# Kernel optimization log

Measured on AMD Instinct MI355X. Metric: run time of the kernel, lower is better.

The kernel has to match this reference:

```python
import jax, jax.numpy as jnp
import numpy as np

N_EMBD = 1024
N_HEAD = 16
B, T = 4, 2048

def setup_inputs() -> dict:
    key = jax.random.key(0)
    ks = jax.random.split(key, 5)
    s_attn = 1.0 / np.sqrt(N_EMBD)
    s_proj = 1.0 / np.sqrt(N_EMBD)
    return {
        "x": jax.random.normal(ks[0], (B, T, N_EMBD), dtype=jnp.float32),
        "w_attn": jax.random.uniform(ks[1], (N_EMBD, 3 * N_EMBD), jnp.float32, -s_attn, s_attn),
        "b_attn": jax.random.uniform(ks[2], (3 * N_EMBD,), jnp.float32, -s_attn, s_attn),
        "w_proj": jax.random.uniform(ks[3], (N_EMBD, N_EMBD), jnp.float32, -s_proj, s_proj),
        "b_proj": jax.random.uniform(ks[4], (N_EMBD,), jnp.float32, -s_proj, s_proj),
    }

def reference(x, w_attn, b_attn, w_proj, b_proj):
    Bx, Tx, C = x.shape
    hd = C // N_HEAD  # head dim
    qkv = x @ w_attn + b_attn                       # [B,T,3C]
    q, k, v = jnp.split(qkv, 3, axis=-1)
    # [B,T,C] -> [B,H,T,hd]
    def heads(t):
        return t.reshape(Bx, Tx, N_HEAD, hd).transpose(0, 2, 1, 3)
    q, k, v = heads(q), heads(k), heads(v)
    att = jnp.einsum('bhqd,bhkd->bhqk', q, k) * (1.0 / np.sqrt(hd))
    causal = jnp.tril(jnp.ones((Tx, Tx), dtype=bool))
    att = jnp.where(causal, att, -jnp.inf)
    att = jax.nn.softmax(att, axis=-1)
    y = jnp.einsum('bhqk,bhkd->bhqd', att, v)       # [B,H,T,hd]
    y = y.transpose(0, 2, 1, 3).reshape(Bx, Tx, C)
    return y @ w_proj + b_proj
```

## Files before the change

### kernel.cpp

```cpp
#include <hip/hip_runtime.h>
#include <cstdint>

typedef unsigned short u16;
typedef short s16x8 __attribute__((ext_vector_type(8)));
typedef short s16x4 __attribute__((ext_vector_type(4)));
typedef float f32x4 __attribute__((ext_vector_type(4)));

#define B_   4
#define T_   2048
#define C_   1024
#define H_   16
#define HD_  64
#define M_   8192
#define N3_  3072

#define QSCALE 0.18033688011112042f

__device__ inline u16 f2b(float f) {
  union { float f; uint32_t u; } v; v.f = f;
  uint32_t u = v.u;
  return (u16)((u + 0x7FFFu + ((u >> 16) & 1u)) >> 16);
}

__device__ inline uint32_t cvtpk(float lo, float hi) {
  uint32_t r;
  asm("v_cvt_pk_bf16_f32 %0, %1, %2" : "=v"(r) : "v"(lo), "v"(hi));
  return r;
}

__device__ inline f32x4 mfma16(s16x4 a, s16x4 b, f32x4 c) {
#if __has_builtin(__builtin_amdgcn_mfma_f32_16x16x16bf16_1k)
  return __builtin_amdgcn_mfma_f32_16x16x16bf16_1k(a, b, c, 0, 0, 0);
#else
  f32x4 d;
  asm("v_mfma_f32_16x16x16_bf16 %0, %1, %2, %3"
      : "=v"(d) : "v"(a), "v"(b), "v"(c));
  return d;
#endif
}

__device__ inline void gload_lds16(const void* g, void* l) {
  __builtin_amdgcn_global_load_lds(
      (const __attribute__((address_space(1))) void*)g,
      (__attribute__((address_space(3))) void*)l, 16, 0, 0);
}

__global__ __launch_bounds__(256) void cvt_f32_bf16(
    const float* __restrict__ in, u16* __restrict__ out, int n) {
  int i = (blockIdx.x * 256 + threadIdx.x) * 8;
  if (i >= n) return;
  float4 a = *(const float4*)(in + i);
  float4 b = *(const float4*)(in + i + 4);
  s16x8 r;
  r[0] = (short)f2b(a.x); r[1] = (short)f2b(a.y);
  r[2] = (short)f2b(a.z); r[3] = (short)f2b(a.w);
  r[4] = (short)f2b(b.x); r[5] = (short)f2b(b.y);
  r[6] = (short)f2b(b.z); r[7] = (short)f2b(b.w);
  *(s16x8*)(out + i) = r;
}

__global__ __launch_bounds__(256) void cvt_transpose(
    const float* __restrict__ W, u16* __restrict__ WT, int K, int N) {
  __shared__ u16 tile[64][65];
  int n0 = blockIdx.x * 64, k0 = blockIdx.y * 64;
  int j = threadIdx.x & 63, i0 = threadIdx.x >> 6;
#pragma unroll
  for (int i = i0; i < 64; i += 4)
    tile[i][j] = f2b(W[(size_t)(k0 + i) * N + n0 + j]);
  __syncthreads();
#pragma unroll
  for (int i = i0; i < 64; i += 4)
    WT[(size_t)(n0 + i) * K + k0 + j] = tile[j][i];
}

template <int MODE>
__global__ __launch_bounds__(256, 4) void gemm_bt(
    const u16* __restrict__ A, const u16* __restrict__ Bt,
    const float* __restrict__ bias, float* __restrict__ outf,
    u16* __restrict__ qo, u16* __restrict__ ko, u16* __restrict__ vo,
    int M, int N, int K) {
  __shared__ u16 As[128 * 64];
  __shared__ u16 Bs[128 * 64];

  int nwg = gridDim.x;
  int bid0 = blockIdx.x;
  int bid = (bid0 & 7) * (nwg >> 3) + (bid0 >> 3);
  int nbn = N >> 7;
  int bm = bid / nbn, bn = bid % nbn;
  int m0 = bm * 128, n0 = bn * 128;
  int tid = threadIdx.x;
  int lane = tid & 63, w = tid >> 6;
  int wm = (w >> 1) * 64, wn = (w & 1) * 64;
  int l15 = lane & 15, g = lane >> 4;

  f32x4 acc[4][4] = {};

  for (int kb = 0; kb < K; kb += 64) {
    __syncthreads();
#pragma unroll
    for (int p = 0; p < 4; ++p) {
      int idx = p * 256 + tid;
      int row = idx >> 3, pc = idx & 7;
      int sc = (pc ^ (row & 7)) * 8;
      gload_lds16(A  + (size_t)(m0 + row) * K + kb + sc, &As[idx * 8]);
      gload_lds16(Bt + (size_t)(n0 + row) * K + kb + sc, &Bs[idx * 8]);
    }
    __syncthreads();

#pragma unroll
    for (int ks = 0; ks < 2; ++ks) {
      int ck = ((g + 4 * ks) ^ (l15 & 7)) * 8;
      s16x8 af[4], bf[4];
#pragma unroll
      for (int mi = 0; mi < 4; ++mi)
        af[mi] = *(const s16x8*)&As[(wm + mi * 16 + l15) * 64 + ck];
#pragma unroll
      for (int ni = 0; ni < 4; ++ni)
        bf[ni] = *(const s16x8*)&Bs[(wn + ni * 16 + l15) * 64 + ck];
#pragma unroll
      for (int mi = 0; mi < 4; ++mi)
#pragma unroll
        for (int ni = 0; ni < 4; ++ni)
          acc[mi][ni] = __builtin_amdgcn_mfma_f32_16x16x32_bf16(
              af[mi], bf[ni], acc[mi][ni], 0, 0, 0);
    }
  }

#pragma unroll
  for (int mi = 0; mi < 4; ++mi)
#pragma unroll
    for (int ni = 0; ni < 4; ++ni) {
      int col = n0 + wn + ni * 16 + l15;
      float bv = bias[col];
      int row0 = m0 + wm + mi * 16 + g * 4;
      if (MODE == 0) {
#pragma unroll
        for (int r = 0; r < 4; ++r)
          outf[(size_t)(row0 + r) * N + col] = acc[mi][ni][r] + bv;
      } else {
        int which = col >> 10, hc = col & 1023;
        int h = hc >> 6, d = hc & 63;
        int b = row0 >> 11, t0 = row0 & 2047;
        if (which == 2) {
          s16x4 pv;
#pragma unroll
          for (int r = 0; r < 4; ++r) pv[r] = (short)f2b(acc[mi][ni][r] + bv);
          *(s16x4*)(vo + ((size_t)((b * 16 + h) * 64 + d)) * 2048 + t0) = pv;
        } else {
          u16* dst = (which == 0) ? qo : ko;
          float sc2 = (which == 0) ? QSCALE : 1.0f;
#pragma unroll
          for (int r = 0; r < 4; ++r)
            dst[(((size_t)(b * 16 + h)) * 2048 + (t0 + r)) * 64 + d] =
                f2b((acc[mi][ni][r] + bv) * sc2);
        }
      }
    }
}

__global__ __launch_bounds__(256, 4) void attn_fwd(
    const u16* __restrict__ Q, const u16* __restrict__ Kg,
    const u16* __restrict__ Vt, u16* __restrict__ Y) {
  __shared__ u16 Ks[64 * 64];
  __shared__ u16 Vs[64 * 64];

  int bid = blockIdx.x;
  int bh = bid & 63;
  int qt = 31 - (bid >> 6);
  int tid = threadIdx.x, lane = tid & 63, w = tid >> 6;
  int l15 = lane & 15, g = lane >> 4;

  const u16* Qh = Q  + (size_t)bh * T_ * HD_;
  const u16* Kh = Kg + (size_t)bh * T_ * HD_;
  const u16* Vh = Vt + (size_t)bh * HD_ * T_;

  int q0 = qt * 64 + w * 16;
  int qrow = q0 + l15;

  s16x8 qa[2];
#pragma unroll
  for (int ks = 0; ks < 2; ++ks)
    qa[ks] = *(const s16x8*)(Qh + (size_t)qrow * HD_ + g * 8 + ks * 32);

  f32x4 oacc[4] = {};
  float m = -3.0e30f, l = 0.f;

  int sr = tid >> 3, sc = tid & 7;
  int wswz = (sr & 7) << 4;
  int rswz = (l15 & 7) << 4;
  char* KsB = (char*)Ks;
  char* VsB = (char*)Vs;

  s16x8 kr0 = *(const s16x8*)(Kh + (size_t)sr * HD_ + sc * 8);
  s16x8 kr1 = *(const s16x8*)(Kh + (size_t)(sr + 32) * HD_ + sc * 8);
  s16x8 vr0 = *(const s16x8*)(Vh + (size_t)sr * T_ + sc * 8);
  s16x8 vr1 = *(const s16x8*)(Vh + (size_t)(sr + 32) * T_ + sc * 8);

  int ntile = qt + 1;
  for (int kt = 0; kt < ntile; ++kt) {
    int kvb = kt * 64;
    __syncthreads();
    *(s16x8*)(KsB + sr * 128 + ((sc * 16) ^ wswz))        = kr0;
    *(s16x8*)(KsB + (sr + 32) * 128 + ((sc * 16) ^ wswz)) = kr1;
    *(s16x8*)(VsB + sr * 128 + ((sc * 16) ^ wswz))        = vr0;
    *(s16x8*)(VsB + (sr + 32) * 128 + ((sc * 16) ^ wswz)) = vr1;
    __syncthreads();

    {
      int kvn = (kt + 1 < ntile) ? (kt + 1) * 64 : 0;
      kr0 = *(const s16x8*)(Kh + (size_t)(kvn + sr) * HD_ + sc * 8);
      kr1 = *(const s16x8*)(Kh + (size_t)(kvn + sr + 32) * HD_ + sc * 8);
      vr0 = *(const s16x8*)(Vh + (size_t)sr * T_ + kvn + sc * 8);
      vr1 = *(const s16x8*)(Vh + (size_t)(sr + 32) * T_ + kvn + sc * 8);
    }

    f32x4 sacc[4] = {};
    __builtin_amdgcn_s_setprio(1);
#pragma unroll
    for (int cf = 0; cf < 4; ++cf)
#pragma unroll
      for (int ks = 0; ks < 2; ++ks) {
        s16x8 kb = *(const s16x8*)(KsB + (cf * 16 + l15) * 128 +
                                   ((g * 16 + ks * 64) ^ rswz));
        sacc[cf] = __builtin_amdgcn_mfma_f32_16x16x32_bf16(kb, qa[ks], sacc[cf], 0, 0, 0);
      }
    __builtin_amdgcn_s_setprio(0);

    if (kt == qt) {
#pragma unroll
      for (int cf = 0; cf < 4; ++cf)
#pragma unroll
        for (int r = 0; r < 4; ++r) {
          int kv = kvb + cf * 16 + g * 4 + r;
          if (kv > qrow) sacc[cf][r] = -1e30f;
        }
    }

    float t0 = fmaxf(fmaxf(sacc[0][0], sacc[0][1]), fmaxf(sacc[0][2], sacc[0][3]));
    float t1 = fmaxf(fmaxf(sacc[1][0], sacc[1][1]), fmaxf(sacc[1][2], sacc[1][3]));
    float t2 = fmaxf(fmaxf(sacc[2][0], sacc[2][1]), fmaxf(sacc[2][2], sacc[2][3]));
    float t3 = fmaxf(fmaxf(sacc[3][0], sacc[3][1]), fmaxf(sacc[3][2], sacc[3][3]));
    float mx = fmaxf(fmaxf(t0, t1), fmaxf(t2, t3));
    mx = fmaxf(mx, __shfl_xor(mx, 16, 64));
    mx = fmaxf(mx, __shfl_xor(mx, 32, 64));

    if (!__all(mx <= m + 8.0f)) {
      float mn = fmaxf(m, mx);
      float alpha = __builtin_amdgcn_exp2f(m - mn);
      m = mn;
      l *= alpha;
#pragma unroll
      for (int df = 0; df < 4; ++df)
#pragma unroll
        for (int r = 0; r < 4; ++r) oacc[df][r] *= alpha;
    }

    float rs = 0.f;
#pragma unroll
    for (int cf = 0; cf < 4; ++cf)
#pragma unroll
      for (int r = 0; r < 4; ++r) {
        float p = __builtin_amdgcn_exp2f(sacc[cf][r] - m);
        sacc[cf][r] = p;
        rs += p;
      }
    rs += __shfl_xor(rs, 16, 64);
    rs += __shfl_xor(rs, 32, 64);
    l += rs;

#pragma unroll
    for (int cf = 0; cf < 4; ++cf) {
      union { uint32_t u[2]; s16x4 v; } pk;
      pk.u[0] = cvtpk(sacc[cf][0], sacc[cf][1]);
      pk.u[1] = cvtpk(sacc[cf][2], sacc[cf][3]);
      __builtin_amdgcn_s_setprio(1);
#pragma unroll
      for (int df = 0; df < 4; ++df) {
        s16x4 va = *(const s16x4*)(VsB + (df * 16 + l15) * 128 +
                                   ((cf * 32 + g * 8) ^ rswz));
        oacc[df] = mfma16(va, pk.v, oacc[df]);
      }
      __builtin_amdgcn_s_setprio(0);
    }
  }

  int b = bh >> 4, h = bh & 15;
  float inv = 1.0f / l;
  u16* yrow = Y + ((size_t)b * T_ + qrow) * C_ + h * 64;
#pragma unroll
  for (int df = 0; df < 4; ++df) {
    union { uint32_t u[2]; s16x4 v; } pk;
    pk.u[0] = cvtpk(oacc[df][0] * inv, oacc[df][1] * inv);
    pk.u[1] = cvtpk(oacc[df][2] * inv, oacc[df][3] * inv);
    *(s16x4*)(yrow + df * 16 + g * 4) = pk.v;
  }
}

extern "C" void kernel_launch(void* const* d_in, const int* in_sizes, int n_in,
                              void* d_out, int out_size, void* d_ws, size_t ws_size,
                              hipStream_t stream) {
  const float* x      = (const float*)d_in[0];
  const float* w_attn = (const float*)d_in[1];
  const float* b_attn = (const float*)d_in[2];
  const float* w_proj = (const float*)d_in[3];
  const float* b_proj = (const float*)d_in[4];
  float* out = (float*)d_out;

  u16* ws  = (u16*)d_ws;
  u16* xb  = ws;
  u16* wat = xb  + (size_t)M_ * C_;
  u16* wpt = wat + (size_t)N3_ * C_;
  u16* q   = wpt + (size_t)C_ * C_;
  u16* k   = q   + (size_t)M_ * C_;
  u16* v   = k   + (size_t)M_ * C_;
  u16* ya  = xb;

  cvt_f32_bf16<<<dim3((M_ * C_) / (256 * 8)), dim3(256), 0, stream>>>(x, xb, M_ * C_);
  cvt_transpose<<<dim3(N3_ / 64, C_ / 64), dim3(256), 0, stream>>>(w_attn, wat, C_, N3_);
  cvt_transpose<<<dim3(C_ / 64, C_ / 64), dim3(256), 0, stream>>>(w_proj, wpt, C_, C_);

  gemm_bt<1><<<dim3((M_ / 128) * (N3_ / 128)), dim3(256), 0, stream>>>(
      xb, wat, b_attn, nullptr, q, k, v, M_, N3_, C_);

  attn_fwd<<<dim3(64 * 32), dim3(256), 0, stream>>>(q, k, v, ya);

  gemm_bt<0><<<dim3((M_ / 128) * (C_ / 128)), dim3(256), 0, stream>>>(
      ya, wpt, b_proj, out, nullptr, nullptr, nullptr, M_, C_, C_);
}
```

Baseline: 186.5 us.

## Switch attention to 32x32x16 MFMA with 128-row query blocks per workgroup

Rewrites the attention kernel so each workgroup handles 128 query rows (32 per wave) instead of 64, and uses 32x32x16 bf16 MFMAs for both QK^T and PV in place of 16x16 variants. Each K/V tile loaded into LDS is therefore reused by twice as many queries, and P is repacked across lane halves with shuffles to form the B operand for PV. Waves whose query rows lie entirely before a KV tile skip its compute. The cost is more accumulator registers (occupancy hint lowered from 4 to 3 workgroups per CU), half as many workgroups, and extra shuffle work per tile.

```diff
diff --git a/kernel.cpp b/kernel.cpp
--- a/kernel.cpp
+++ b/kernel.cpp
@@ -5,6 +5,7 @@
 typedef short s16x8 __attribute__((ext_vector_type(8)));
 typedef short s16x4 __attribute__((ext_vector_type(4)));
 typedef float f32x4 __attribute__((ext_vector_type(4)));
+typedef float f32x16 __attribute__((ext_vector_type(16)));
 
 #define B_   4
 #define T_   2048
@@ -26,17 +27,6 @@
   uint32_t r;
   asm("v_cvt_pk_bf16_f32 %0, %1, %2" : "=v"(r) : "v"(lo), "v"(hi));
   return r;
-}
-
-__device__ inline f32x4 mfma16(s16x4 a, s16x4 b, f32x4 c) {
-#if __has_builtin(__builtin_amdgcn_mfma_f32_16x16x16bf16_1k)
-  return __builtin_amdgcn_mfma_f32_16x16x16bf16_1k(a, b, c, 0, 0, 0);
-#else
-  f32x4 d;
-  asm("v_mfma_f32_16x16x16_bf16 %0, %1, %2, %3"
-      : "=v"(d) : "v"(a), "v"(b), "v"(c));
-  return d;
-#endif
 }
 
 __device__ inline void gload_lds16(const void* g, void* l) {
@@ -158,7 +148,7 @@
     }
 }
 
-__global__ __launch_bounds__(256, 4) void attn_fwd(
+__global__ __launch_bounds__(256, 3) void attn_fwd(
     const u16* __restrict__ Q, const u16* __restrict__ Kg,
     const u16* __restrict__ Vt, u16* __restrict__ Y) {
   __shared__ u16 Ks[64 * 64];
@@ -166,28 +156,29 @@
 
   int bid = blockIdx.x;
   int bh = bid & 63;
-  int qt = 31 - (bid >> 6);
+  int qb = 15 - (bid >> 6);
   int tid = threadIdx.x, lane = tid & 63, w = tid >> 6;
-  int l15 = lane & 15, g = lane >> 4;
+  int l31 = lane & 31, half = lane >> 5;
 
   const u16* Qh = Q  + (size_t)bh * T_ * HD_;
   const u16* Kh = Kg + (size_t)bh * T_ * HD_;
   const u16* Vh = Vt + (size_t)bh * HD_ * T_;
 
-  int q0 = qt * 64 + w * 16;
-  int qrow = q0 + l15;
-
-  s16x8 qa[2];
-#pragma unroll
-  for (int ks = 0; ks < 2; ++ks)
-    qa[ks] = *(const s16x8*)(Qh + (size_t)qrow * HD_ + g * 8 + ks * 32);
-
-  f32x4 oacc[4] = {};
+  int q0 = qb * 128;
+  int qw = q0 + w * 32;
+  int qrow = qw + l31;
+
+  s16x8 qa[4];
+#pragma unroll
+  for (int kst = 0; kst < 4; ++kst)
+    qa[kst] = *(const s16x8*)(Qh + (size_t)qrow * HD_ + kst * 16 + half * 8);
+
+  f32x16 oacc[2] = {};
   float m = -3.0e30f, l = 0.f;
 
   int sr = tid >> 3, sc = tid & 7;
   int wswz = (sr & 7) << 4;
-  int rswz = (l15 & 7) << 4;
+  int rswz = (l31 & 7) << 4;
   char* KsB = (char*)Ks;
   char* VsB = (char*)Vs;
 
@@ -196,7 +187,7 @@
   s16x8 vr0 = *(const s16x8*)(Vh + (size_t)sr * T_ + sc * 8);
   s16x8 vr1 = *(const s16x8*)(Vh + (size_t)(sr + 32) * T_ + sc * 8);
 
-  int ntile = qt + 1;
+  int ntile = 2 * qb + 2;
   for (int kt = 0; kt < ntile; ++kt) {
     int kvb = kt * 64;
     __syncthreads();
@@ -214,34 +205,40 @@
       vr1 = *(const s16x8*)(Vh + (size_t)(sr + 32) * T_ + kvn + sc * 8);
     }
 
-    f32x4 sacc[4] = {};
+    if (kvb > qw + 31) continue;
+
+    f32x16 s0 = {}, s1 = {};
     __builtin_amdgcn_s_setprio(1);
 #pragma unroll
-    for (int cf = 0; cf < 4; ++cf)
-#pragma unroll
-      for (int ks = 0; ks < 2; ++ks) {
-        s16x8 kb = *(const s16x8*)(KsB + (cf * 16 + l15) * 128 +
-                                   ((g * 16 + ks * 64) ^ rswz));
-        sacc[cf] = __builtin_amdgcn_mfma_f32_16x16x32_bf16(kb, qa[ks], sacc[cf], 0, 0, 0);
+    for (int kst = 0; kst < 4; ++kst) {
+      s16x8 kb0 = *(const s16x8*)(KsB +
+          (((l31) * 128 + kst * 32 + half * 16) ^ rswz));
+      s0 = __builtin_amdgcn_mfma_f32_32x32x16_bf16(kb0, qa[kst], s0, 0, 0, 0);
+      s16x8 kb1 = *(const s16x8*)(KsB +
+          (((32 + l31) * 128 + kst * 32 + half * 16) ^ rswz));
+      s1 = __builtin_amdgcn_mfma_f32_32x32x16_bf16(kb1, qa[kst], s1, 0, 0, 0);
+    }
+    __builtin_amdgcn_s_setprio(0);
+
+    if (kvb + 63 > qw) {
+#pragma unroll
+      for (int r = 0; r < 16; ++r) {
+        int kv0 = kvb + (r & 3) + 8 * (r >> 2) + 4 * half;
+        if (kv0 > qrow) s0[r] = -1e30f;
+        if (kv0 + 32 > qrow) s1[r] = -1e30f;
       }
-    __builtin_amdgcn_s_setprio(0);
-
-    if (kt == qt) {
-#pragma unroll
-      for (int cf = 0; cf < 4; ++cf)
-#pragma unroll
-        for (int r = 0; r < 4; ++r) {
-          int kv = kvb + cf * 16 + g * 4 + r;
-          if (kv > qrow) sacc[cf][r] = -1e30f;
-        }
-    }
-
-    float t0 = fmaxf(fmaxf(sacc[0][0], sacc[0][1]), fmaxf(sacc[0][2], sacc[0][3]));
-    float t1 = fmaxf(fmaxf(sacc[1][0], sacc[1][1]), fmaxf(sacc[1][2], sacc[1][3]));
-    float t2 = fmaxf(fmaxf(sacc[2][0], sacc[2][1]), fmaxf(sacc[2][2], sacc[2][3]));
-    float t3 = fmaxf(fmaxf(sacc[3][0], sacc[3][1]), fmaxf(sacc[3][2], sacc[3][3]));
-    float mx = fmaxf(fmaxf(t0, t1), fmaxf(t2, t3));
-    mx = fmaxf(mx, __shfl_xor(mx, 16, 64));
+    }
+
+    float a0 = fmaxf(fmaxf(s0[0], s0[1]), fmaxf(s0[2], s0[3]));
+    float a1 = fmaxf(fmaxf(s0[4], s0[5]), fmaxf(s0[6], s0[7]));
+    float a2 = fmaxf(fmaxf(s0[8], s0[9]), fmaxf(s0[10], s0[11]));
+    float a3 = fmaxf(fmaxf(s0[12], s0[13]), fmaxf(s0[14], s0[15]));
+    float a4 = fmaxf(fmaxf(s1[0], s1[1]), fmaxf(s1[2], s1[3]));
+    float a5 = fmaxf(fmaxf(s1[4], s1[5]), fmaxf(s1[6], s1[7]));
+    float a6 = fmaxf(fmaxf(s1[8], s1[9]), fmaxf(s1[10], s1[11]));
+    float a7 = fmaxf(fmaxf(s1[12], s1[13]), fmaxf(s1[14], s1[15]));
+    float mx = fmaxf(fmaxf(fmaxf(a0, a1), fmaxf(a2, a3)),
+                     fmaxf(fmaxf(a4, a5), fmaxf(a6, a7)));
     mx = fmaxf(mx, __shfl_xor(mx, 32, 64));
 
     if (!__all(mx <= m + 8.0f)) {
@@ -250,50 +247,64 @@
       m = mn;
       l *= alpha;
 #pragma unroll
-      for (int df = 0; df < 4; ++df)
-#pragma unroll
-        for (int r = 0; r < 4; ++r) oacc[df][r] *= alpha;
+      for (int i = 0; i < 16; ++i) { oacc[0][i] *= alpha; oacc[1][i] *= alpha; }
     }
 
     float rs = 0.f;
 #pragma unroll
-    for (int cf = 0; cf < 4; ++cf)
-#pragma unroll
-      for (int r = 0; r < 4; ++r) {
-        float p = __builtin_amdgcn_exp2f(sacc[cf][r] - m);
-        sacc[cf][r] = p;
-        rs += p;
-      }
-    rs += __shfl_xor(rs, 16, 64);
+    for (int r = 0; r < 16; ++r) {
+      float p0 = __builtin_amdgcn_exp2f(s0[r] - m);
+      float p1 = __builtin_amdgcn_exp2f(s1[r] - m);
+      s0[r] = p0; s1[r] = p1;
+      rs += p0 + p1;
+    }
     rs += __shfl_xor(rs, 32, 64);
     l += rs;
 
-#pragma unroll
-    for (int cf = 0; cf < 4; ++cf) {
-      union { uint32_t u[2]; s16x4 v; } pk;
-      pk.u[0] = cvtpk(sacc[cf][0], sacc[cf][1]);
-      pk.u[1] = cvtpk(sacc[cf][2], sacc[cf][3]);
-      __builtin_amdgcn_s_setprio(1);
-#pragma unroll
-      for (int df = 0; df < 4; ++df) {
-        s16x4 va = *(const s16x4*)(VsB + (df * 16 + l15) * 128 +
-                                   ((cf * 32 + g * 8) ^ rswz));
-        oacc[df] = mfma16(va, pk.v, oacc[df]);
+    s16x8 pb[4];
+#pragma unroll
+    for (int ks4 = 0; ks4 < 4; ++ks4) {
+      const f32x16& sv = (ks4 < 2) ? s0 : s1;
+      const int R = (ks4 & 1) * 8;
+      uint32_t A0 = cvtpk(sv[R + 0], sv[R + 1]);
+      uint32_t A1 = cvtpk(sv[R + 2], sv[R + 3]);
+      uint32_t B0 = cvtpk(sv[R + 4], sv[R + 5]);
+      uint32_t B1 = cvtpk(sv[R + 6], sv[R + 7]);
+      uint32_t r0 = (uint32_t)__shfl_xor((int)(half ? A0 : B0), 32, 64);
+      uint32_t r1 = (uint32_t)__shfl_xor((int)(half ? A1 : B1), 32, 64);
+      union { uint32_t u[4]; s16x8 v; } pk_;
+      pk_.u[0] = half ? r0 : A0;
+      pk_.u[1] = half ? r1 : A1;
+      pk_.u[2] = half ? B0 : r0;
+      pk_.u[3] = half ? B1 : r1;
+      pb[ks4] = pk_.v;
+    }
+
+    __builtin_amdgcn_s_setprio(1);
+#pragma unroll
+    for (int hb = 0; hb < 2; ++hb)
+#pragma unroll
+      for (int ks4 = 0; ks4 < 4; ++ks4) {
+        s16x8 va = *(const s16x8*)(VsB +
+            (((hb * 32 + l31) * 128 + ks4 * 32 + half * 16) ^ rswz));
+        oacc[hb] = __builtin_amdgcn_mfma_f32_32x32x16_bf16(va, pb[ks4],
+                                                           oacc[hb], 0, 0, 0);
       }
-      __builtin_amdgcn_s_setprio(0);
-    }
+    __builtin_amdgcn_s_setprio(0);
   }
 
   int b = bh >> 4, h = bh & 15;
   float inv = 1.0f / l;
   u16* yrow = Y + ((size_t)b * T_ + qrow) * C_ + h * 64;
 #pragma unroll
-  for (int df = 0; df < 4; ++df) {
-    union { uint32_t u[2]; s16x4 v; } pk;
-    pk.u[0] = cvtpk(oacc[df][0] * inv, oacc[df][1] * inv);
-    pk.u[1] = cvtpk(oacc[df][2] * inv, oacc[df][3] * inv);
-    *(s16x4*)(yrow + df * 16 + g * 4) = pk.v;
-  }
+  for (int hb = 0; hb < 2; ++hb)
+#pragma unroll
+    for (int rg = 0; rg < 4; ++rg) {
+      union { uint32_t u[2]; s16x4 v; } o;
+      o.u[0] = cvtpk(oacc[hb][rg * 4 + 0] * inv, oacc[hb][rg * 4 + 1] * inv);
+      o.u[1] = cvtpk(oacc[hb][rg * 4 + 2] * inv, oacc[hb][rg * 4 + 3] * inv);
+      *(s16x4*)(yrow + hb * 32 + rg * 8 + half * 4) = o.v;
+    }
 }
 
 extern "C" void kernel_launch(void* const* d_in, const int* in_sizes, int n_in,
@@ -322,7 +333,7 @@
   gemm_bt<1><<<dim3((M_ / 128) * (N3_ / 128)), dim3(256), 0, stream>>>(
       xb, wat, b_attn, nullptr, q, k, v, M_, N3_, C_);
 
-  attn_fwd<<<dim3(64 * 32), dim3(256), 0, stream>>>(q, k, v, ya);
+  attn_fwd<<<dim3(64 * 16), dim3(256), 0, stream>>>(q, k, v, ya);
 
   gemm_bt<0><<<dim3((M_ / 128) * (C_ / 128)), dim3(256), 0, stream>>>(
       ya, wpt, b_proj, out, nullptr, nullptr, nullptr, M_, C_, C_);
```

Result: faster. 166.5 us (-10.8%).
